# Optimization experiments

Measured on AMD Instinct MI355X. Metric: run time of the kernel, lower is better.

## Reference

```python
import jax, jax.numpy as jnp
import numpy as np

NUM_HEADS = 16


def setup_inputs() -> dict:
    key = jax.random.key(0)
    ks = jax.random.split(key, 5)
    B, S, H = 2, 2048, 1024
    scale = 0.02
    return {
        "x": jax.random.normal(ks[0], (B, S, H), dtype=jnp.float32),
        "w_qkv": jax.random.normal(ks[1], (H, 3 * H), dtype=jnp.float32) * scale,
        "b_qkv": jax.random.normal(ks[2], (3 * H,), dtype=jnp.float32) * scale,
        "w_out": jax.random.normal(ks[3], (H, H), dtype=jnp.float32) * scale,
        "b_out": jax.random.normal(ks[4], (H,), dtype=jnp.float32) * scale,
    }


def reference(x, w_qkv, b_qkv, w_out, b_out):
    B, S, H = x.shape
    nh = NUM_HEADS
    hd = H // nh
    attn_scale = 1.0 / np.sqrt(hd).astype(np.float32)

    qkv = x @ w_qkv + b_qkv                       # (B, S, 3H)
    q, k, v = jnp.split(qkv, 3, axis=-1)
    # (B, S, H) -> (B, nh, S, hd)
    to_heads = lambda t: t.reshape(B, S, nh, hd).transpose(0, 2, 1, 3)
    q, k, v = to_heads(q), to_heads(k), to_heads(v)

    scores = jnp.einsum("bhid,bhjd->bhij", q, k) * attn_scale  # (B, nh, S, S)
    # Source masks where triu(ones)==0 -> strictly-lower triangle masked;
    # allowed positions are j >= i (attends to present and future).
    i = jnp.arange(S)[:, None]
    j = jnp.arange(S)[None, :]
    scores = jnp.where(j >= i, scores, -jnp.inf)
    attn = jax.nn.softmax(scores, axis=-1)        # dropout is identity (eval)

    out = jnp.einsum("bhij,bhjd->bhid", attn, v)  # (B, nh, S, hd)
    out = out.transpose(0, 2, 1, 3).reshape(B, S, H)
    return out @ w_out + b_out
```

## Files before the change

kernel.cpp:

```cpp
#include <hip/hip_runtime.h>
#include <hip/hip_bf16.h>
#include <stdint.h>
#include <stddef.h>

typedef __bf16 bf16_t;
typedef __bf16 bf16x4 __attribute__((ext_vector_type(4)));
typedef __bf16 bf16x8 __attribute__((ext_vector_type(8)));
typedef float f32x4 __attribute__((ext_vector_type(4)));
typedef float f32x16 __attribute__((ext_vector_type(16)));

#define MFMA16(a, b, c) __builtin_amdgcn_mfma_f32_16x16x32_bf16(a, b, c, 0, 0, 0)
#define MFMA32(a, b, c) __builtin_amdgcn_mfma_f32_32x32x16_bf16(a, b, c, 0, 0, 0)

#define GLL16(g, l)                                                      \
    __builtin_amdgcn_global_load_lds(                                    \
        (const __attribute__((address_space(1))) void*)(g),              \
        (__attribute__((address_space(3))) void*)(l), 16, 0, 0)

#define SEQ 2048
#define NHEAD 16
#define HD 64
#define HID 1024
#define QKV_LD 3072
#define VT_LD 2080

__global__ __launch_bounds__(256)
void prep_kernel(const float* __restrict__ x, const float* __restrict__ w_qkv,
                 const float* __restrict__ w_out, bf16_t* __restrict__ xbf,
                 bf16_t* __restrict__ wqkvT, bf16_t* __restrict__ woutT) {
    int L = blockIdx.x;
    int tid = threadIdx.x;
    if (L < 4096) {
        int i = (L * 256 + tid) * 4;
        float4 v = *(const float4*)(x + i);
        bf16x4 o = {(bf16_t)v.x, (bf16_t)v.y, (bf16_t)v.z, (bf16_t)v.w};
        *(bf16x4*)(xbf + i) = o;
        return;
    }
    __shared__ bf16_t tile[32][33];
    const float* W;
    bf16_t* Wt;
    int N, bx, by;
    if (L < 7168) {
        int r = L - 4096;
        W = w_qkv; Wt = wqkvT; N = 3072; bx = r % 96; by = r / 96;
    } else {
        int r = L - 7168;
        W = w_out; Wt = woutT; N = 1024; bx = r % 32; by = r / 32;
    }
    int K = 1024;
    int n0 = bx * 32, k0 = by * 32;
    int tx = tid & 31, ty = tid >> 5;
#pragma unroll
    for (int i = 0; i < 4; i++)
        tile[ty + i * 8][tx] = (bf16_t)W[(size_t)(k0 + ty + i * 8) * N + n0 + tx];
    __syncthreads();
#pragma unroll
    for (int i = 0; i < 4; i++)
        Wt[(size_t)(n0 + ty + i * 8) * K + k0 + tx] = tile[tx][ty + i * 8];
}

__global__ __launch_bounds__(256)
void vt_transpose(const bf16_t* __restrict__ qkv, bf16_t* __restrict__ Vt) {
    int s0 = blockIdx.x * 64;
    int bh = blockIdx.y;
    int b = bh >> 4, h = bh & 15;
    int tid = threadIdx.x;
    __shared__ __align__(16) bf16_t tile[64][72];

    int row = tid >> 3, c8 = (tid & 7) * 8;
#pragma unroll
    for (int it = 0; it < 2; it++) {
        int sr = row + it * 32;
        bf16x8 v = *(const bf16x8*)(qkv + ((size_t)b * SEQ + s0 + sr) * QKV_LD +
                                    2 * HID + h * HD + c8);
        *(bf16x8*)(&tile[sr][c8]) = v;
    }
    __syncthreads();
#pragma unroll
    for (int it = 0; it < 2; it++) {
        int d = row + it * 32;
        bf16x8 w;
#pragma unroll
        for (int e = 0; e < 8; e++) w[e] = tile[c8 + e][d];
        *(bf16x8*)(Vt + ((size_t)bh * HD + d) * VT_LD + s0 + c8) = w;
    }
}

template <typename OutT, int TN>
__global__ __launch_bounds__(256)
void gemm_bt_bias(const bf16_t* __restrict__ A, const bf16_t* __restrict__ Bt,
                  const float* __restrict__ bias, OutT* __restrict__ C,
                  int M, int N, int K) {
    constexpr int NT = TN / 32;
    __shared__ __align__(16) bf16_t As[128][32];
    __shared__ __align__(16) bf16_t Bs[TN][32];

    int m0 = blockIdx.y * 128;
    int n0 = blockIdx.x * TN;
    int tid = threadIdx.x;
    int wave = tid >> 6, lane = tid & 63;
    int quad = lane >> 4, l16 = lane & 15;
    int wm = (wave >> 1) * 64, wn = (wave & 1) * (TN / 2);

    f32x4 acc[4][NT] = {};

    const bf16_t* a_base =
        A + (size_t)(m0 + wave * 32 + (lane >> 2)) * K + (lane & 3) * 8;
    const bf16_t* b_base =
        Bt + (size_t)(n0 + wave * (TN / 4) + (lane >> 2)) * K + (lane & 3) * 8;
    bf16_t* as_base = &As[wave * 32][0];
    bf16_t* bs_base = &Bs[wave * (TN / 4)][0];

    for (int k0 = 0; k0 < K; k0 += 32) {
        GLL16(a_base + k0, as_base);
        GLL16(a_base + 16 * K + k0, as_base + 16 * 32);
        GLL16(b_base + k0, bs_base);
        if (TN == 128) GLL16(b_base + 16 * K + k0, bs_base + 16 * 32);
        __syncthreads();

        bf16x8 af[4], bfr[NT];
#pragma unroll
        for (int t = 0; t < 4; t++)
            af[t] = *(const bf16x8*)(&As[wm + t * 16 + l16][quad * 8]);
#pragma unroll
        for (int t = 0; t < NT; t++)
            bfr[t] = *(const bf16x8*)(&Bs[wn + t * 16 + l16][quad * 8]);
#pragma unroll
        for (int mt = 0; mt < 4; mt++)
#pragma unroll
            for (int nt = 0; nt < NT; nt++)
                acc[mt][nt] = MFMA16(af[mt], bfr[nt], acc[mt][nt]);
        __syncthreads();
    }

#pragma unroll
    for (int mt = 0; mt < 4; mt++) {
        int row = m0 + wm + mt * 16 + quad * 4;
#pragma unroll
        for (int nt = 0; nt < NT; nt++) {
            int col = n0 + wn + nt * 16 + l16;
            float bv = bias[col];
#pragma unroll
            for (int r = 0; r < 4; r++)
                C[(size_t)(row + r) * N + col] = (OutT)(acc[mt][nt][r] + bv);
        }
    }
}

__global__ __launch_bounds__(256)
void attn_kernel(const bf16_t* __restrict__ qkv, const bf16_t* __restrict__ Vt,
                 bf16_t* __restrict__ attn_out) {
    int bh = blockIdx.x;
    int tile = blockIdx.y;
    int b = bh >> 4, h = bh & 15;

    int tid = threadIdx.x, wave = tid >> 6, lane = tid & 63;
    int l32 = lane & 31, hi = lane >> 5;
    int ih = wave & 1, jh = wave >> 1;

    const bf16_t* q_g = qkv + (size_t)b * SEQ * QKV_LD + (size_t)h * HD;
    const bf16_t* k_g = q_g + HID;
    const bf16_t* vt_g = Vt + (size_t)bh * HD * VT_LD;

    __shared__ __align__(16) bf16_t Ks[64][72];
    __shared__ __align__(16) bf16_t Vs[64][72];
    __shared__ __align__(16) bf16_t Ps[64][68];
    __shared__ float lsumS[4][32];

    const float QS = 0.125f * 1.44269504088896f;
    int i0 = tile * 64;

    bf16x8 qa[4];
    {
        const bf16_t* qrow = q_g + (size_t)(i0 + ih * 32 + l32) * QKV_LD + hi * 8;
#pragma unroll
        for (int ks = 0; ks < 4; ks++) {
            bf16x8 t = *(const bf16x8*)(qrow + ks * 16);
#pragma unroll
            for (int e = 0; e < 8; e++) qa[ks][e] = (bf16_t)((float)t[e] * QS);
        }
    }

    f32x16 o = {};
    float lsum = 0.0f;

    int sr = tid >> 2, sc = (tid & 3) * 8;

    bf16x8 kr[2], vr[2];
#pragma unroll
    for (int t = 0; t < 2; t++) {
        kr[t] = *(const bf16x8*)(k_g + (size_t)(i0 + sr) * QKV_LD + sc + t * 32);
        vr[t] = *(const bf16x8*)(vt_g + (size_t)sr * VT_LD + i0 + sc + t * 32);
    }

    for (int j0 = i0; j0 < SEQ; j0 += 64) {
        __syncthreads();
#pragma unroll
        for (int t = 0; t < 2; t++) {
            *(bf16x8*)(&Ks[sr][sc + t * 32]) = kr[t];
            *(bf16x8*)(&Vs[sr][sc + t * 32]) = vr[t];
        }
        __syncthreads();

        if (j0 + 64 < SEQ) {
#pragma unroll
            for (int t = 0; t < 2; t++) {
                kr[t] = *(const bf16x8*)(k_g + (size_t)(j0 + 64 + sr) * QKV_LD + sc + t * 32);
                vr[t] = *(const bf16x8*)(vt_g + (size_t)sr * VT_LD + j0 + 64 + sc + t * 32);
            }
        }

        f32x16 st = {};
#pragma unroll
        for (int ks = 0; ks < 4; ks++) {
            bf16x8 ka = *(const bf16x8*)(&Ks[jh * 32 + l32][ks * 16 + hi * 8]);
            st = MFMA32(ka, qa[ks], st);
        }

        if (j0 == i0) {
            int gi = i0 + ih * 32 + l32;
#pragma unroll
            for (int rq = 0; rq < 4; rq++) {
                bf16x4 pk;
#pragma unroll
                for (int r = 0; r < 4; r++) {
                    int gj = j0 + jh * 32 + 8 * rq + 4 * hi + r;
                    float p = (gj >= gi) ? __builtin_amdgcn_exp2f(st[rq * 4 + r]) : 0.0f;
                    lsum += p;
                    pk[r] = (bf16_t)p;
                }
                *(bf16x4*)(&Ps[ih * 32 + l32][jh * 32 + 8 * rq + 4 * hi]) = pk;
            }
        } else {
#pragma unroll
            for (int rq = 0; rq < 4; rq++) {
                bf16x4 pk;
#pragma unroll
                for (int r = 0; r < 4; r++) {
                    float p = __builtin_amdgcn_exp2f(st[rq * 4 + r]);
                    lsum += p;
                    pk[r] = (bf16_t)p;
                }
                *(bf16x4*)(&Ps[ih * 32 + l32][jh * 32 + 8 * rq + 4 * hi]) = pk;
            }
        }
        __syncthreads();

#pragma unroll
        for (int ks = 0; ks < 4; ks++) {
            bf16x8 pa = *(const bf16x8*)(&Ps[ih * 32 + l32][ks * 16 + hi * 8]);
            bf16x8 vb = *(const bf16x8*)(&Vs[jh * 32 + l32][ks * 16 + hi * 8]);
            o = MFMA32(pa, vb, o);
        }
    }

    lsum += __shfl_xor(lsum, 32, 64);
    lsumS[wave][l32] = lsum;
    __syncthreads();

#pragma unroll
    for (int rq = 0; rq < 4; rq++) {
#pragma unroll
        for (int r = 0; r < 4; r++) {
            int il = 8 * rq + 4 * hi + r;
            float rs = lsumS[ih][il] + lsumS[ih + 2][il];
            int gi = i0 + ih * 32 + il;
            attn_out[(size_t)(b * SEQ + gi) * HID + h * HD + jh * 32 + l32] =
                (bf16_t)(o[rq * 4 + r] / rs);
        }
    }
}

extern "C" void kernel_launch(void* const* d_in, const int* in_sizes, int n_in,
                              void* d_out, int out_size, void* d_ws, size_t ws_size,
                              hipStream_t stream) {
    const float* x     = (const float*)d_in[0];
    const float* w_qkv = (const float*)d_in[1];
    const float* b_qkv = (const float*)d_in[2];
    const float* w_out = (const float*)d_in[3];
    const float* b_out = (const float*)d_in[4];
    float* out = (float*)d_out;

    char* ws = (char*)d_ws;
    bf16_t* xbf   = (bf16_t*)(ws);
    bf16_t* Vt    = (bf16_t*)(ws);
    bf16_t* wqkvT = (bf16_t*)(ws + 8388608);
    bf16_t* woutT = (bf16_t*)(ws + 14680064);
    bf16_t* qkv   = (bf16_t*)(ws + 16777216);
    bf16_t* attn  = (bf16_t*)(ws + 41943040);

    prep_kernel<<<8192, 256, 0, stream>>>(x, w_qkv, w_out, xbf, wqkvT, woutT);

    gemm_bt_bias<bf16_t, 128><<<dim3(3072 / 128, 4096 / 128), 256, 0, stream>>>(
        xbf, wqkvT, b_qkv, qkv, 4096, 3072, 1024);

    vt_transpose<<<dim3(SEQ / 64, 2 * NHEAD), 256, 0, stream>>>(qkv, Vt);

    attn_kernel<<<dim3(2 * NHEAD, SEQ / 64), 256, 0, stream>>>(qkv, Vt, attn);

    gemm_bt_bias<float, 64><<<dim3(1024 / 64, 4096 / 128), 256, 0, stream>>>(
        attn, woutT, b_out, out, 4096, 1024, 1024);
}
```

Before: 183.2 us.

## Replace QKV GEMM with 256x256-tile, 8-wave, phase-pipelined kernel

Adds a new QKV projection GEMM that uses 256x256 output tiles, 512 threads, and double-buffered LDS filled by direct global-to-LDS loads. The loads are XOR-swizzled and split into four half-tile stages interleaved with four MFMA phases per K step. Workgroup IDs are remapped for better L2 locality, and the MFMA phases run at raised wave priority. The aim is to overlap global loads with math and raise operand reuse compared with the old 128x128 tile GEMM. The cost is 128 KB of LDS per block, many barriers, and only 192 workgroups, which may leave CUs underfilled.

New measurement: 181.6 us. About the same (-0.8%).

```diff
diff --git a/kernel.cpp b/kernel.cpp
--- a/kernel.cpp
+++ b/kernel.cpp
@@ -87,6 +87,172 @@
     }
 }
 
+#define STAGE8(GB, LB, KOFF)                                                   \
+    do {                                                                       \
+        GLL16((GB) + (size_t)srow * K + (KOFF) + ssw,                          \
+              (LB) + srow * 64 + (scl << 3));                                  \
+        GLL16((GB) + (size_t)(srow + 64) * K + (KOFF) + ssw,                   \
+              (LB) + (srow + 64) * 64 + (scl << 3));                           \
+    } while (0)
+
+__global__ __launch_bounds__(512, 2)
+void gemm_qkv_8ph(const bf16_t* __restrict__ A, const bf16_t* __restrict__ Bt,
+                  const float* __restrict__ bias, bf16_t* __restrict__ C,
+                  int M, int N, int K) {
+    __shared__ __align__(16) bf16_t As[2][256][64];
+    __shared__ __align__(16) bf16_t Bs[2][256][64];
+
+    int nbx = N >> 8;
+    int bid = blockIdx.x;
+    int swz = (bid & 7) * (gridDim.x >> 3) + (bid >> 3);
+    int m0 = (swz / nbx) << 8;
+    int n0 = (swz % nbx) << 8;
+
+    int tid = threadIdx.x;
+    int lane = tid & 63;
+    int wave = tid >> 6;
+    int l16 = lane & 15, quad = lane >> 4;
+    int wm = (wave >> 2) << 7;
+    int wn = (wave & 3) << 6;
+
+    int srow = tid >> 3;
+    int scl = tid & 7;
+    int ssw = ((scl ^ (srow & 7)) << 3);
+
+    const bf16_t* Ab = A + (size_t)m0 * K;
+    const bf16_t* Bb = Bt + (size_t)n0 * K;
+
+    f32x4 acc[8][4] = {};
+    bf16x8 af[4][2], b0[2][2], b1[2][2];
+
+    const int NT = K >> 6;
+
+    STAGE8(Bb, &Bs[0][0][0], 0);
+    STAGE8(Ab, &As[0][0][0], 0);
+    STAGE8(Bb + (size_t)128 * K, &Bs[0][128][0], 0);
+    STAGE8(Ab + (size_t)128 * K, &As[0][128][0], 0);
+    STAGE8(Bb, &Bs[1][0][0], 64);
+    STAGE8(Ab, &As[1][0][0], 64);
+    asm volatile("s_waitcnt vmcnt(4)" ::: "memory");
+    __builtin_amdgcn_s_barrier();
+
+    for (int t = 0; t < NT; t++) {
+        int buf = t & 1;
+        const bf16_t* Asb = &As[buf][0][0];
+        const bf16_t* Bsb = &Bs[buf][0][0];
+        int k1 = (t + 1) << 6;
+        int k2 = (t + 2) << 6;
+
+#pragma unroll
+        for (int mt = 0; mt < 4; mt++) {
+            int row = wm + mt * 16 + l16;
+#pragma unroll
+            for (int ks = 0; ks < 2; ks++)
+                af[mt][ks] = *(const bf16x8*)(
+                    Asb + row * 64 + (((ks * 4 + quad) ^ (row & 7)) << 3));
+        }
+#pragma unroll
+        for (int nt = 0; nt < 2; nt++) {
+            int row = wn + nt * 16 + l16;
+#pragma unroll
+            for (int ks = 0; ks < 2; ks++)
+                b0[nt][ks] = *(const bf16x8*)(
+                    Bsb + row * 64 + (((ks * 4 + quad) ^ (row & 7)) << 3));
+        }
+        if (t + 1 < NT) STAGE8(Bb + (size_t)128 * K, &Bs[buf ^ 1][128][0], k1);
+        __builtin_amdgcn_s_barrier();
+        asm volatile("s_waitcnt lgkmcnt(0)" ::: "memory");
+        __builtin_amdgcn_s_setprio(1);
+#pragma unroll
+        for (int mt = 0; mt < 4; mt++)
+#pragma unroll
+            for (int nt = 0; nt < 2; nt++)
+#pragma unroll
+                for (int ks = 0; ks < 2; ks++)
+                    acc[mt][nt] = MFMA16(af[mt][ks], b0[nt][ks], acc[mt][nt]);
+        __builtin_amdgcn_s_setprio(0);
+        __builtin_amdgcn_s_barrier();
+
+#pragma unroll
+        for (int nt = 0; nt < 2; nt++) {
+            int row = wn + 32 + nt * 16 + l16;
+#pragma unroll
+            for (int ks = 0; ks < 2; ks++)
+                b1[nt][ks] = *(const bf16x8*)(
+                    Bsb + row * 64 + (((ks * 4 + quad) ^ (row & 7)) << 3));
+        }
+        if (t + 1 < NT) STAGE8(Ab + (size_t)128 * K, &As[buf ^ 1][128][0], k1);
+        __builtin_amdgcn_s_barrier();
+        asm volatile("s_waitcnt lgkmcnt(0)" ::: "memory");
+        __builtin_amdgcn_s_setprio(1);
+#pragma unroll
+        for (int mt = 0; mt < 4; mt++)
+#pragma unroll
+            for (int nt = 0; nt < 2; nt++)
+#pragma unroll
+                for (int ks = 0; ks < 2; ks++)
+                    acc[mt][2 + nt] =
+                        MFMA16(af[mt][ks], b1[nt][ks], acc[mt][2 + nt]);
+        __builtin_amdgcn_s_setprio(0);
+        __builtin_amdgcn_s_barrier();
+
+#pragma unroll
+        for (int mt = 0; mt < 4; mt++) {
+            int row = wm + 64 + mt * 16 + l16;
+#pragma unroll
+            for (int ks = 0; ks < 2; ks++)
+                af[mt][ks] = *(const bf16x8*)(
+                    Asb + row * 64 + (((ks * 4 + quad) ^ (row & 7)) << 3));
+        }
+        if (t + 2 < NT) STAGE8(Bb, &Bs[buf][0][0], k2);
+        __builtin_amdgcn_s_barrier();
+        asm volatile("s_waitcnt lgkmcnt(0)" ::: "memory");
+        __builtin_amdgcn_s_setprio(1);
+#pragma unroll
+        for (int mt = 0; mt < 4; mt++)
+#pragma unroll
+            for (int nt = 0; nt < 2; nt++)
+#pragma unroll
+                for (int ks = 0; ks < 2; ks++)
+                    acc[4 + mt][nt] =
+                        MFMA16(af[mt][ks], b0[nt][ks], acc[4 + mt][nt]);
+        __builtin_amdgcn_s_setprio(0);
+        __builtin_amdgcn_s_barrier();
+
+        if (t + 2 < NT) {
+            STAGE8(Ab, &As[buf][0][0], k2);
+            asm volatile("s_waitcnt vmcnt(4)" ::: "memory");
+        } else if (t + 1 < NT) {
+            asm volatile("s_waitcnt vmcnt(0)" ::: "memory");
+        }
+        __builtin_amdgcn_s_barrier();
+        __builtin_amdgcn_s_setprio(1);
+#pragma unroll
+        for (int mt = 0; mt < 4; mt++)
+#pragma unroll
+            for (int nt = 0; nt < 2; nt++)
+#pragma unroll
+                for (int ks = 0; ks < 2; ks++)
+                    acc[4 + mt][2 + nt] =
+                        MFMA16(af[mt][ks], b1[nt][ks], acc[4 + mt][2 + nt]);
+        __builtin_amdgcn_s_setprio(0);
+        __builtin_amdgcn_s_barrier();
+    }
+
+#pragma unroll
+    for (int mi = 0; mi < 8; mi++) {
+        int row = m0 + wm + (mi >> 2) * 64 + (mi & 3) * 16 + quad * 4;
+#pragma unroll
+        for (int ni = 0; ni < 4; ni++) {
+            int col = n0 + wn + (ni >> 1) * 32 + (ni & 1) * 16 + l16;
+            float bv = bias[col];
+#pragma unroll
+            for (int r = 0; r < 4; r++)
+                C[(size_t)(row + r) * N + col] = (bf16_t)(acc[mi][ni][r] + bv);
+        }
+    }
+}
+
 template <typename OutT, int TN>
 __global__ __launch_bounds__(256)
 void gemm_bt_bias(const bf16_t* __restrict__ A, const bf16_t* __restrict__ Bt,
@@ -292,8 +458,8 @@
 
     prep_kernel<<<8192, 256, 0, stream>>>(x, w_qkv, w_out, xbf, wqkvT, woutT);
 
-    gemm_bt_bias<bf16_t, 128><<<dim3(3072 / 128, 4096 / 128), 256, 0, stream>>>(
-        xbf, wqkvT, b_qkv, qkv, 4096, 3072, 1024);
+    gemm_qkv_8ph<<<192, 512, 0, stream>>>(xbf, wqkvT, b_qkv, qkv,
+                                          4096, 3072, 1024);
 
     vt_transpose<<<dim3(SEQ / 64, 2 * NHEAD), 256, 0, stream>>>(qkv, Vt);
 
```
